# Performance work log

Hardware: AMD Instinct MI355X
Metric: run time of the kernel (lower is better)

Reference implementation:

```python
import jax, jax.numpy as jnp
import numpy as np

B, N, DK, DV = 16, 4096, 64, 64


def setup_inputs() -> dict:
    key = jax.random.key(0)
    kq, kk, kv = jax.random.split(key, 3)
    q = jax.random.normal(kq, (B, N, DK), dtype=jnp.float32)
    k = jax.random.normal(kk, (B, N, DK), dtype=jnp.float32)
    v = jax.random.normal(kv, (B, N, DV), dtype=jnp.float32)
    # causal mask: positions j<=i are attendable (mask==True)
    mask = jnp.tril(jnp.ones((N, N), dtype=bool))[None, :, :]  # (1, N, N)
    return {"q": q, "k": k, "v": v, "mask": mask}


def reference(q, k, v, mask):
    # scores: (B, N, N)
    scale = 1.0 / jnp.sqrt(jnp.asarray(q.shape[-1], dtype=q.dtype))
    scores = jnp.einsum('bnd,bmd->bnm', q, k) * scale
    scores = jnp.where(mask, scores, jnp.asarray(-jnp.inf, dtype=scores.dtype))
    attn = jax.nn.softmax(scores, axis=-1)
    # dropout is identity in eval/reference mode
    return jnp.einsum('bnm,bmd->bnd', attn, v)
```

## Files before the change

### kernel.cpp

```cpp
#include <hip/hip_runtime.h>


#define N_SEQ 4096
#define DIM   64

typedef __bf16  bf16x8 __attribute__((ext_vector_type(8)));
typedef unsigned short u16x8 __attribute__((ext_vector_type(8)));
typedef float   f32x4  __attribute__((ext_vector_type(4)));
typedef short   short4v __attribute__((ext_vector_type(4)));

static __device__ __forceinline__ unsigned short f2bf(float f) {
    unsigned int u = __float_as_uint(f);
    u += 0x7FFFu + ((u >> 16) & 1u);
    return (unsigned short)(u >> 16);
}

static __device__ __forceinline__ unsigned int pk2bf(float a, float b) {
#if defined(__HIP_DEVICE_COMPILE__) && __has_builtin(__builtin_amdgcn_cvt_pk_bf16_f32)
    typedef __bf16 bf16x2_t __attribute__((ext_vector_type(2)));
    bf16x2_t r = __builtin_amdgcn_cvt_pk_bf16_f32(a, b);
    return __builtin_bit_cast(unsigned int, r);
#else
    return (unsigned int)f2bf(a) | ((unsigned int)f2bf(b) << 16);
#endif
}

static __device__ __forceinline__ float fexp2(float x) {
#if defined(__HIP_DEVICE_COMPILE__) && __has_builtin(__builtin_amdgcn_exp2f)
    return __builtin_amdgcn_exp2f(x);
#else
    return exp2f(x);
#endif
}

static __device__ __forceinline__ bf16x8 ld_frag(const void* p) {
    u16x8 u = *reinterpret_cast<const u16x8*>(p);
    return __builtin_bit_cast(bf16x8, u);
}

static __device__ __forceinline__ f32x4 mfma_pv(uint2 a, uint2 b, f32x4 c) {
#if defined(__HIP_DEVICE_COMPILE__)
#if __has_builtin(__builtin_amdgcn_mfma_f32_16x16x16bf16_1k)
    return __builtin_amdgcn_mfma_f32_16x16x16bf16_1k(
        __builtin_bit_cast(short4v, a), __builtin_bit_cast(short4v, b), c, 0, 0, 0);
#else
    f32x4 d;
    asm volatile("v_mfma_f32_16x16x16_bf16 %0, %1, %2, %3"
                 : "=v"(d) : "v"(a), "v"(b), "v"(c));
    return d;
#endif
#else
    (void)a; (void)b;
    return c;
#endif
}

static __device__ __forceinline__ void gl_lds16(const unsigned short* g, unsigned short* l) {
#if defined(__HIP_DEVICE_COMPILE__)
    __builtin_amdgcn_global_load_lds(
        (const __attribute__((address_space(1))) unsigned int*)(g),
        (__attribute__((address_space(3))) unsigned int*)(l), 16, 0, 0);
#else
    (void)g; (void)l;
#endif
}

__global__ __launch_bounds__(256)
void prep_kv(const float* __restrict__ K, const float* __restrict__ V,
             unsigned short* __restrict__ wsK, unsigned short* __restrict__ wsV) {
    const int b = blockIdx.y, t = blockIdx.x;
    if (blockIdx.z == 0) {
        const float* src = K + ((size_t)b * N_SEQ + t * 64) * DIM;
        unsigned short* dst = wsK + ((size_t)(b * 64 + t)) * 4096;
        #pragma unroll
        for (int ph = 0; ph < 2; ++ph) {
            const int gidx = threadIdx.x + ph * 256;
            const int r = gidx >> 3, g = gidx & 7;
            const float* p = src + r * DIM + g * 8;
            f32x4 f0 = *reinterpret_cast<const f32x4*>(p);
            f32x4 f1 = *reinterpret_cast<const f32x4*>(p + 4);
            uint4 w;
            w.x = pk2bf(f0[0], f0[1]); w.y = pk2bf(f0[2], f0[3]);
            w.z = pk2bf(f1[0], f1[1]); w.w = pk2bf(f1[2], f1[3]);
            *reinterpret_cast<uint4*>(&dst[(r * 8 + (g ^ (r & 7))) * 8]) = w;
        }
    } else {
        const int dv = threadIdx.x & 63;
        const int g0 = threadIdx.x >> 6;
        const float* src = V + ((size_t)b * N_SEQ + t * 64) * DIM + dv;
        unsigned short* dst = wsV + ((size_t)(b * 64 + t)) * 4096;
        #pragma unroll
        for (int ph = 0; ph < 2; ++ph) {
            const int gp = g0 + ph * 4;
            float p[8];
            #pragma unroll
            for (int e = 0; e < 8; ++e) {
                const int pos = gp * 8 + e;
                const int kp  = ((pos >> 2) & 3) * 16 + (pos >> 4) * 4 + (pos & 3);
                p[e] = src[(size_t)kp * DIM];
            }
            uint4 w;
            w.x = pk2bf(p[0], p[1]); w.y = pk2bf(p[2], p[3]);
            w.z = pk2bf(p[4], p[5]); w.w = pk2bf(p[6], p[7]);
            *reinterpret_cast<uint4*>(&dst[(dv * 8 + (gp ^ (dv & 7))) * 8]) = w;
        }
    }
}

__global__ __launch_bounds__(256)
void attn_fwd(const float* __restrict__ Q, const unsigned short* __restrict__ wsK,
              const unsigned short* __restrict__ wsV, float* __restrict__ O,
              float* __restrict__ wsO, float* __restrict__ wsL) {
    __shared__ unsigned short kbuf[2][4096];
    __shared__ unsigned short vbuf[2][4096];

    const int tid  = threadIdx.x;
    const int wave = tid >> 6;
    const int lane = tid & 63;
    const int quad = lane >> 4;
    const int ln   = lane & 15;
    const int ln7  = lane & 7;

    const int L    = (int)blockIdx.x;
    const int r    = L & 7;
    const int w    = L >> 3;
    const int role = w & 1;
    const int bsel = (w >> 1) & 1;
    const int j    = w >> 2;
    const int b    = r * 2 + bsel;
    const int T    = 63 - j;

    int it_tile[2], it_k0[2], it_k1[2], it_half[2], n_items;
    if (role == 0) {
        it_tile[0] = j;  it_k0[0] = 0; it_k1[0] = j + 1;  it_half[0] = -1;
        it_tile[1] = T;  it_k0[1] = 0; it_k1[1] = 31 - j; it_half[1] = 0;
        n_items = 2;
    } else {
        it_tile[0] = T;  it_k0[0] = 31 - j; it_k1[0] = 64 - j; it_half[0] = 1;
        n_items = 1;
    }

    int kaddr[2][4];
    #pragma unroll
    for (int s = 0; s < 2; ++s)
        #pragma unroll
        for (int nt = 0; nt < 4; ++nt)
            kaddr[s][nt] = (nt * 16 + ln) * 128 + (((s * 4 + quad) ^ ln7) * 16);
    int vaddr[2][4];
    #pragma unroll
    for (int c = 0; c < 2; ++c)
        #pragma unroll
        for (int dvt = 0; dvt < 4; ++dvt)
            vaddr[c][dvt] = (dvt * 16 + ln) * 128 + ((((quad << 1) | c) ^ ln7) * 16);

    const int dma_off = wave * 1024 + lane * 8;
    const uint2 ones  = make_uint2(0x3F803F80u, 0x3F803F80u);
    const float QS = 0.125f * 1.44269504f;

    const unsigned short* kt_src = wsK + (size_t)b * 64 * 4096;
    const unsigned short* vt_src = wsV + (size_t)b * 64 * 4096;

    for (int it = 0; it < n_items; ++it) {
        const int tt   = it_tile[it];
        const int kt0  = it_k0[it];
        const int kt1  = it_k1[it];
        const int half = it_half[it];
        const int i0   = tt * 64;
        const int qloc = i0 + wave * 16 + ln;

        __syncthreads();

        f32x4 o_acc[4] = {};
        f32x4 lacc = {};

        if (kt0 < kt1) {
            const float* qptr = Q + ((size_t)b * N_SEQ + i0 + wave * 16 + ln) * DIM;
            u16x8 qa[2];
            #pragma unroll
            for (int s = 0; s < 2; ++s) {
                const float* p = qptr + s * 32 + quad * 8;
                f32x4 f0 = *reinterpret_cast<const f32x4*>(p);
                f32x4 f1 = *reinterpret_cast<const f32x4*>(p + 4);
                #pragma unroll
                for (int jj = 0; jj < 4; ++jj) {
                    qa[s][jj]     = f2bf(f0[jj] * QS);
                    qa[s][4 + jj] = f2bf(f1[jj] * QS);
                }
            }

            auto dma = [&](int kt, int bufi) {
                const unsigned short* ks = kt_src + (size_t)kt * 4096 + dma_off;
                const unsigned short* vs = vt_src + (size_t)kt * 4096 + dma_off;
                #pragma unroll
                for (int i = 0; i < 2; ++i) {
                    gl_lds16(ks + i * 512, &kbuf[bufi][wave * 1024 + i * 512]);
                    gl_lds16(vs + i * 512, &vbuf[bufi][wave * 1024 + i * 512]);
                }
            };

            auto compute = [&](int kt, const unsigned short* kb, const unsigned short* vb) {
                f32x4 st[4] = {};
                #pragma unroll
                for (int s = 0; s < 2; ++s) {
                    bf16x8 qf = __builtin_bit_cast(bf16x8, qa[s]);
                    #pragma unroll
                    for (int nt = 0; nt < 4; ++nt) {
                        bf16x8 kf = ld_frag((const char*)kb + kaddr[s][nt]);
                        st[nt] = __builtin_amdgcn_mfma_f32_16x16x32_bf16(kf, qf, st[nt], 0, 0, 0);
                    }
                }
                uint2 pk_d[4];
                if (kt == tt) {
                    const int kbase = kt * 64 + quad * 4;
                    #pragma unroll
                    for (int nt = 0; nt < 4; ++nt) {
                        const int kp = kbase + nt * 16;
                        float p0 = fexp2((kp + 0 > qloc) ? -3.0e38f : st[nt][0]);
                        float p1 = fexp2((kp + 1 > qloc) ? -3.0e38f : st[nt][1]);
                        float p2 = fexp2((kp + 2 > qloc) ? -3.0e38f : st[nt][2]);
                        float p3 = fexp2((kp + 3 > qloc) ? -3.0e38f : st[nt][3]);
                        pk_d[nt].x = pk2bf(p0, p1);
                        pk_d[nt].y = pk2bf(p2, p3);
                    }
                } else {
                    #pragma unroll
                    for (int nt = 0; nt < 4; ++nt) {
                        pk_d[nt].x = pk2bf(fexp2(st[nt][0]), fexp2(st[nt][1]));
                        pk_d[nt].y = pk2bf(fexp2(st[nt][2]), fexp2(st[nt][3]));
                    }
                }
                #pragma unroll
                for (int c = 0; c < 2; ++c)
                    #pragma unroll
                    for (int dvt = 0; dvt < 4; ++dvt) {
                        uint4 bv = *reinterpret_cast<const uint4*>(
                            (const char*)vb + vaddr[c][dvt]);
                        o_acc[dvt] = mfma_pv(pk_d[2 * c],     make_uint2(bv.x, bv.y), o_acc[dvt]);
                        o_acc[dvt] = mfma_pv(pk_d[2 * c + 1], make_uint2(bv.z, bv.w), o_acc[dvt]);
                    }
                #pragma unroll
                for (int nt = 0; nt < 4; ++nt)
                    lacc = mfma_pv(pk_d[nt], ones, lacc);
            };

            dma(kt0, 0);
            int kt = kt0, bufi = 0;
            while (true) {
                __syncthreads();
                if (kt + 1 < kt1) dma(kt + 1, bufi ^ 1);
                compute(kt, kbuf[bufi], vbuf[bufi]);
                if (++kt == kt1) break;
                bufi ^= 1;
            }
        }

        if (half < 0) {
            float* obase = O + ((size_t)b * N_SEQ + i0 + wave * 16) * DIM;
            #pragma unroll
            for (int rr = 0; rr < 4; ++rr) {
                const float inv = 1.0f / lacc[rr];
                #pragma unroll
                for (int dvt = 0; dvt < 4; ++dvt)
                    obase[(quad * 4 + rr) * DIM + dvt * 16 + ln] = o_acc[dvt][rr] * inv;
            }
        } else {
            float* po = wsO + (((size_t)(b * 32 + (tt - 32)) * 2 + half) * 4096)
                      + (wave * 16) * 64;
            float* pl = wsL + (((size_t)(b * 32 + (tt - 32)) * 2 + half) * 64)
                      + wave * 16;
            #pragma unroll
            for (int rr = 0; rr < 4; ++rr) {
                #pragma unroll
                for (int dvt = 0; dvt < 4; ++dvt)
                    po[(quad * 4 + rr) * 64 + dvt * 16 + ln] = o_acc[dvt][rr];
                if (ln == 0) pl[quad * 4 + rr] = lacc[rr];
            }
        }
    }
}

__global__ __launch_bounds__(256)
void norm_out(const float* __restrict__ wsO, const float* __restrict__ wsL,
              float* __restrict__ O) {
    const int t = 32 + blockIdx.x, b = blockIdx.y;
    const int row = threadIdx.x >> 2;
    const int c0  = (threadIdx.x & 3) * 16;
    const size_t base = (size_t)(b * 32 + (t - 32)) * 2;
    const float* p0 = wsO + base * 4096 + row * 64 + c0;
    const float* p1 = p0 + 4096;
    const float* l  = wsL + base * 64;
    const float inv = 1.0f / (l[row] + l[64 + row]);
    float* o = O + ((size_t)b * N_SEQ + t * 64 + row) * 64 + c0;
    #pragma unroll
    for (int i = 0; i < 16; i += 4) {
        f32x4 a = *reinterpret_cast<const f32x4*>(p0 + i);
        f32x4 c = *reinterpret_cast<const f32x4*>(p1 + i);
        f32x4 v = (a + c) * inv;
        *reinterpret_cast<f32x4*>(o + i) = v;
    }
}

extern "C" void kernel_launch(void* const* d_in, const int* in_sizes, int n_in,
                              void* d_out, int out_size, void* d_ws, size_t ws_size,
                              hipStream_t stream) {
    const float* q = (const float*)d_in[0];
    const float* k = (const float*)d_in[1];
    const float* v = (const float*)d_in[2];
    float* out = (float*)d_out;

    unsigned short* wsK = (unsigned short*)d_ws;
    unsigned short* wsV = wsK + (size_t)16 * 64 * 4096;
    float* wsO = (float*)(wsV + (size_t)16 * 64 * 4096);
    float* wsL = wsO + (size_t)16 * 32 * 2 * 4096;

    prep_kv<<<dim3(64, 16, 2), dim3(256), 0, stream>>>(k, v, wsK, wsV);
    attn_fwd<<<dim3(1024), dim3(256), 0, stream>>>(q, wsK, wsV, out, wsO, wsL);
    norm_out<<<dim3(32, 16), dim3(256), 0, stream>>>(wsO, wsL, out);
}
```

Baseline: 193.5 us.

## Split attention tile across waves as 2x2 query/key grid with LDS reduction

Rather than each wave owning 16 query rows against all 64 keys, the four waves form a 2x2 grid: each handles 32 query rows against 32 keys of the tile. Each K fragment loaded from LDS now feeds two MFMAs, and V fragments are halved in size. The V workspace layout and swizzle are changed to match. The partial outputs and row sums from the two key-halves are combined through LDS at the end. This adds two barriers and an LDS reduction per item, and a launch bound hint of 4 blocks per CU constrains registers.

```diff
diff --git a/kernel.cpp b/kernel.cpp
--- a/kernel.cpp
+++ b/kernel.cpp
@@ -88,26 +88,26 @@
         const int dv = threadIdx.x & 63;
         const int g0 = threadIdx.x >> 6;
         const float* src = V + ((size_t)b * N_SEQ + t * 64) * DIM + dv;
-        unsigned short* dst = wsV + ((size_t)(b * 64 + t)) * 4096;
+        unsigned short* dst = wsV + ((size_t)(b * 64 + t)) * 4096 + dv * 64;
         #pragma unroll
         for (int ph = 0; ph < 2; ++ph) {
-            const int gp = g0 + ph * 4;
-            float p[8];
             #pragma unroll
-            for (int e = 0; e < 8; ++e) {
-                const int pos = gp * 8 + e;
-                const int kp  = ((pos >> 2) & 3) * 16 + (pos >> 4) * 4 + (pos & 3);
-                p[e] = src[(size_t)kp * DIM];
+            for (int h = 0; h < 2; ++h) {
+                const int m = g0 * 4 + ph * 2 + h;
+                const float p0 = src[(size_t)(m * 4 + 0) * DIM];
+                const float p1 = src[(size_t)(m * 4 + 1) * DIM];
+                const float p2 = src[(size_t)(m * 4 + 2) * DIM];
+                const float p3 = src[(size_t)(m * 4 + 3) * DIM];
+                uint2 wv;
+                wv.x = pk2bf(p0, p1);
+                wv.y = pk2bf(p2, p3);
+                *reinterpret_cast<uint2*>(&dst[(m ^ (dv & 15)) * 4]) = wv;
             }
-            uint4 w;
-            w.x = pk2bf(p[0], p[1]); w.y = pk2bf(p[2], p[3]);
-            w.z = pk2bf(p[4], p[5]); w.w = pk2bf(p[6], p[7]);
-            *reinterpret_cast<uint4*>(&dst[(dv * 8 + (gp ^ (dv & 7))) * 8]) = w;
         }
     }
 }
 
-__global__ __launch_bounds__(256)
+__global__ __launch_bounds__(256, 4)
 void attn_fwd(const float* __restrict__ Q, const unsigned short* __restrict__ wsK,
               const unsigned short* __restrict__ wsV, float* __restrict__ O,
               float* __restrict__ wsO, float* __restrict__ wsL) {
@@ -120,6 +120,8 @@
     const int quad = lane >> 4;
     const int ln   = lane & 15;
     const int ln7  = lane & 7;
+    const int wq   = wave & 1;
+    const int wk   = wave >> 1;
 
     const int L    = (int)blockIdx.x;
     const int r    = L & 7;
@@ -140,18 +142,19 @@
         n_items = 1;
     }
 
-    int kaddr[2][4];
+    int kaddr[2][2];
     #pragma unroll
     for (int s = 0; s < 2; ++s)
         #pragma unroll
-        for (int nt = 0; nt < 4; ++nt)
-            kaddr[s][nt] = (nt * 16 + ln) * 128 + (((s * 4 + quad) ^ ln7) * 16);
+        for (int nt = 0; nt < 2; ++nt)
+            kaddr[s][nt] = (wk * 32 + nt * 16 + ln) * 128 + (((s * 4 + quad) ^ ln7) * 16);
     int vaddr[2][4];
     #pragma unroll
-    for (int c = 0; c < 2; ++c)
+    for (int nt = 0; nt < 2; ++nt)
         #pragma unroll
         for (int dvt = 0; dvt < 4; ++dvt)
-            vaddr[c][dvt] = (dvt * 16 + ln) * 128 + ((((quad << 1) | c) ^ ln7) * 16);
+            vaddr[nt][dvt] = (dvt * 16 + ln) * 128
+                           + ((((wk * 8 + nt * 4 + quad) ^ ln) & 15) * 8);
 
     const int dma_off = wave * 1024 + lane * 8;
     const uint2 ones  = make_uint2(0x3F803F80u, 0x3F803F80u);
@@ -166,27 +169,28 @@
         const int kt1  = it_k1[it];
         const int half = it_half[it];
         const int i0   = tt * 64;
-        const int qloc = i0 + wave * 16 + ln;
 
         __syncthreads();
 
-        f32x4 o_acc[4] = {};
-        f32x4 lacc = {};
+        f32x4 o_part[2][4] = {};
+        f32x4 lacc[2] = {};
 
         if (kt0 < kt1) {
-            const float* qptr = Q + ((size_t)b * N_SEQ + i0 + wave * 16 + ln) * DIM;
-            u16x8 qa[2];
+            u16x8 qa[2][2];
+            const float* qptr = Q + ((size_t)b * N_SEQ + i0 + wq * 32 + ln) * DIM + quad * 8;
             #pragma unroll
-            for (int s = 0; s < 2; ++s) {
-                const float* p = qptr + s * 32 + quad * 8;
-                f32x4 f0 = *reinterpret_cast<const f32x4*>(p);
-                f32x4 f1 = *reinterpret_cast<const f32x4*>(p + 4);
-                #pragma unroll
-                for (int jj = 0; jj < 4; ++jj) {
-                    qa[s][jj]     = f2bf(f0[jj] * QS);
-                    qa[s][4 + jj] = f2bf(f1[jj] * QS);
-                }
-            }
+            for (int qt = 0; qt < 2; ++qt)
+                #pragma unroll
+                for (int s = 0; s < 2; ++s) {
+                    const float* p = qptr + (size_t)(qt * 16) * DIM + s * 32;
+                    f32x4 f0 = *reinterpret_cast<const f32x4*>(p);
+                    f32x4 f1 = *reinterpret_cast<const f32x4*>(p + 4);
+                    #pragma unroll
+                    for (int jj = 0; jj < 4; ++jj) {
+                        qa[s][qt][jj]     = f2bf(f0[jj] * QS);
+                        qa[s][qt][4 + jj] = f2bf(f1[jj] * QS);
+                    }
+                }
 
             auto dma = [&](int kt, int bufi) {
                 const unsigned short* ks = kt_src + (size_t)kt * 4096 + dma_off;
@@ -199,48 +203,55 @@
             };
 
             auto compute = [&](int kt, const unsigned short* kb, const unsigned short* vb) {
-                f32x4 st[4] = {};
+                f32x4 st[2][2] = {};
                 #pragma unroll
                 for (int s = 0; s < 2; ++s) {
-                    bf16x8 qf = __builtin_bit_cast(bf16x8, qa[s]);
-                    #pragma unroll
-                    for (int nt = 0; nt < 4; ++nt) {
-                        bf16x8 kf = ld_frag((const char*)kb + kaddr[s][nt]);
-                        st[nt] = __builtin_amdgcn_mfma_f32_16x16x32_bf16(kf, qf, st[nt], 0, 0, 0);
-                    }
-                }
-                uint2 pk_d[4];
+                    bf16x8 kf0 = ld_frag((const char*)kb + kaddr[s][0]);
+                    bf16x8 kf1 = ld_frag((const char*)kb + kaddr[s][1]);
+                    #pragma unroll
+                    for (int qt = 0; qt < 2; ++qt) {
+                        bf16x8 qf = __builtin_bit_cast(bf16x8, qa[s][qt]);
+                        st[0][qt] = __builtin_amdgcn_mfma_f32_16x16x32_bf16(kf0, qf, st[0][qt], 0, 0, 0);
+                        st[1][qt] = __builtin_amdgcn_mfma_f32_16x16x32_bf16(kf1, qf, st[1][qt], 0, 0, 0);
+                    }
+                }
+                uint2 pA[2][2];
                 if (kt == tt) {
-                    const int kbase = kt * 64 + quad * 4;
-                    #pragma unroll
-                    for (int nt = 0; nt < 4; ++nt) {
-                        const int kp = kbase + nt * 16;
-                        float p0 = fexp2((kp + 0 > qloc) ? -3.0e38f : st[nt][0]);
-                        float p1 = fexp2((kp + 1 > qloc) ? -3.0e38f : st[nt][1]);
-                        float p2 = fexp2((kp + 2 > qloc) ? -3.0e38f : st[nt][2]);
-                        float p3 = fexp2((kp + 3 > qloc) ? -3.0e38f : st[nt][3]);
-                        pk_d[nt].x = pk2bf(p0, p1);
-                        pk_d[nt].y = pk2bf(p2, p3);
+                    #pragma unroll
+                    for (int nt = 0; nt < 2; ++nt) {
+                        const int kbase = wk * 32 + nt * 16 + quad * 4;
+                        #pragma unroll
+                        for (int qt = 0; qt < 2; ++qt) {
+                            const int qrel = wq * 32 + qt * 16 + ln;
+                            float p0 = fexp2((kbase + 0 > qrel) ? -3.0e38f : st[nt][qt][0]);
+                            float p1 = fexp2((kbase + 1 > qrel) ? -3.0e38f : st[nt][qt][1]);
+                            float p2 = fexp2((kbase + 2 > qrel) ? -3.0e38f : st[nt][qt][2]);
+                            float p3 = fexp2((kbase + 3 > qrel) ? -3.0e38f : st[nt][qt][3]);
+                            pA[nt][qt].x = pk2bf(p0, p1);
+                            pA[nt][qt].y = pk2bf(p2, p3);
+                        }
                     }
                 } else {
                     #pragma unroll
-                    for (int nt = 0; nt < 4; ++nt) {
-                        pk_d[nt].x = pk2bf(fexp2(st[nt][0]), fexp2(st[nt][1]));
-                        pk_d[nt].y = pk2bf(fexp2(st[nt][2]), fexp2(st[nt][3]));
-                    }
-                }
-                #pragma unroll
-                for (int c = 0; c < 2; ++c)
+                    for (int nt = 0; nt < 2; ++nt)
+                        #pragma unroll
+                        for (int qt = 0; qt < 2; ++qt) {
+                            pA[nt][qt].x = pk2bf(fexp2(st[nt][qt][0]), fexp2(st[nt][qt][1]));
+                            pA[nt][qt].y = pk2bf(fexp2(st[nt][qt][2]), fexp2(st[nt][qt][3]));
+                        }
+                }
+                #pragma unroll
+                for (int nt = 0; nt < 2; ++nt) {
                     #pragma unroll
                     for (int dvt = 0; dvt < 4; ++dvt) {
-                        uint4 bv = *reinterpret_cast<const uint4*>(
-                            (const char*)vb + vaddr[c][dvt]);
-                        o_acc[dvt] = mfma_pv(pk_d[2 * c],     make_uint2(bv.x, bv.y), o_acc[dvt]);
-                        o_acc[dvt] = mfma_pv(pk_d[2 * c + 1], make_uint2(bv.z, bv.w), o_acc[dvt]);
-                    }
-                #pragma unroll
-                for (int nt = 0; nt < 4; ++nt)
-                    lacc = mfma_pv(pk_d[nt], ones, lacc);
+                        uint2 bv = *reinterpret_cast<const uint2*>(
+                            (const char*)vb + vaddr[nt][dvt]);
+                        o_part[0][dvt] = mfma_pv(pA[nt][0], bv, o_part[0][dvt]);
+                        o_part[1][dvt] = mfma_pv(pA[nt][1], bv, o_part[1][dvt]);
+                    }
+                    lacc[0] = mfma_pv(pA[nt][0], ones, lacc[0]);
+                    lacc[1] = mfma_pv(pA[nt][1], ones, lacc[1]);
+                }
             };
 
             dma(kt0, 0);
@@ -254,26 +265,62 @@
             }
         }
 
-        if (half < 0) {
-            float* obase = O + ((size_t)b * N_SEQ + i0 + wave * 16) * DIM;
+        __syncthreads();
+        float* red  = reinterpret_cast<float*>(&kbuf[0][0]);
+        float* lred = reinterpret_cast<float*>(&vbuf[0][0]);
+        if (wk == 1) {
             #pragma unroll
-            for (int rr = 0; rr < 4; ++rr) {
-                const float inv = 1.0f / lacc[rr];
+            for (int qt = 0; qt < 2; ++qt) {
                 #pragma unroll
                 for (int dvt = 0; dvt < 4; ++dvt)
-                    obase[(quad * 4 + rr) * DIM + dvt * 16 + ln] = o_acc[dvt][rr] * inv;
+                    #pragma unroll
+                    for (int rr = 0; rr < 4; ++rr)
+                        red[wq * 2048 + qt * 1024 + (quad * 4 + rr) * 64 + dvt * 16 + ln]
+                            = o_part[qt][dvt][rr];
+                if (ln == 0) {
+                    #pragma unroll
+                    for (int rr = 0; rr < 4; ++rr)
+                        lred[wq * 32 + qt * 16 + quad * 4 + rr] = lacc[qt][rr];
+                }
             }
-        } else {
-            float* po = wsO + (((size_t)(b * 32 + (tt - 32)) * 2 + half) * 4096)
-                      + (wave * 16) * 64;
-            float* pl = wsL + (((size_t)(b * 32 + (tt - 32)) * 2 + half) * 64)
-                      + wave * 16;
+        }
+        __syncthreads();
+        if (wk == 0) {
             #pragma unroll
-            for (int rr = 0; rr < 4; ++rr) {
+            for (int qt = 0; qt < 2; ++qt) {
+                f32x4 lt;
+                #pragma unroll
+                for (int rr = 0; rr < 4; ++rr)
+                    lt[rr] = lacc[qt][rr] + lred[wq * 32 + qt * 16 + quad * 4 + rr];
                 #pragma unroll
                 for (int dvt = 0; dvt < 4; ++dvt)
-                    po[(quad * 4 + rr) * 64 + dvt * 16 + ln] = o_acc[dvt][rr];
-                if (ln == 0) pl[quad * 4 + rr] = lacc[rr];
+                    #pragma unroll
+                    for (int rr = 0; rr < 4; ++rr)
+                        o_part[qt][dvt][rr]
+                            += red[wq * 2048 + qt * 1024 + (quad * 4 + rr) * 64 + dvt * 16 + ln];
+
+                const int row0 = wq * 32 + qt * 16 + quad * 4;
+                if (half < 0) {
+                    float* obase = O + ((size_t)b * N_SEQ + i0 + row0) * DIM;
+                    #pragma unroll
+                    for (int rr = 0; rr < 4; ++rr) {
+                        const float inv = 1.0f / lt[rr];
+                        #pragma unroll
+                        for (int dvt = 0; dvt < 4; ++dvt)
+                            obase[rr * DIM + dvt * 16 + ln] = o_part[qt][dvt][rr] * inv;
+                    }
+                } else {
+                    float* po = wsO + (((size_t)(b * 32 + (tt - 32)) * 2 + half) * 4096)
+                              + row0 * 64;
+                    float* pl = wsL + (((size_t)(b * 32 + (tt - 32)) * 2 + half) * 64) + row0;
+                    #pragma unroll
+                    for (int rr = 0; rr < 4; ++rr) {
+                        #pragma unroll
+                        for (int dvt = 0; dvt < 4; ++dvt)
+                            po[rr * 64 + dvt * 16 + ln] = o_part[qt][dvt][rr];
+                        if (ln == 0) pl[rr] = lt[rr];
+                    }
+                }
             }
         }
     }
```

Measured after the change: 196.2 us. About the same (+1.4%).

## Switch attention to 32x32x16 MFMA with 2x2 wave split and LDS reduction

Applied to the files above, without the earlier changes.

Replaces the 16x16 MFMA tiling with 32x32x16 bf16 MFMAs. The four waves now split the 64x64 tile as two query halves times two key halves, and a final LDS reduction combines the key-half partial outputs and row sums. The K/V prep layouts are permuted to match the new fragment addressing, and launch bounds are set to four blocks per CU. The aim is fewer MFMA issues and fewer LDS fragment loads per tile, at the cost of an extra cross-wave reduction with two barriers and higher register pressure from the 16-wide accumulators.

```diff
diff --git a/kernel.cpp b/kernel.cpp
--- a/kernel.cpp
+++ b/kernel.cpp
@@ -7,7 +7,7 @@
 typedef __bf16  bf16x8 __attribute__((ext_vector_type(8)));
 typedef unsigned short u16x8 __attribute__((ext_vector_type(8)));
 typedef float   f32x4  __attribute__((ext_vector_type(4)));
-typedef short   short4v __attribute__((ext_vector_type(4)));
+typedef float   f32x16 __attribute__((ext_vector_type(16)));
 
 static __device__ __forceinline__ unsigned short f2bf(float f) {
     unsigned int u = __float_as_uint(f);
@@ -38,14 +38,13 @@
     return __builtin_bit_cast(bf16x8, u);
 }
 
-static __device__ __forceinline__ f32x4 mfma_pv(uint2 a, uint2 b, f32x4 c) {
+static __device__ __forceinline__ f32x16 mfma32(bf16x8 a, bf16x8 b, f32x16 c) {
 #if defined(__HIP_DEVICE_COMPILE__)
-#if __has_builtin(__builtin_amdgcn_mfma_f32_16x16x16bf16_1k)
-    return __builtin_amdgcn_mfma_f32_16x16x16bf16_1k(
-        __builtin_bit_cast(short4v, a), __builtin_bit_cast(short4v, b), c, 0, 0, 0);
-#else
-    f32x4 d;
-    asm volatile("v_mfma_f32_16x16x16_bf16 %0, %1, %2, %3"
+#if __has_builtin(__builtin_amdgcn_mfma_f32_32x32x16_bf16)
+    return __builtin_amdgcn_mfma_f32_32x32x16_bf16(a, b, c, 0, 0, 0);
+#else
+    f32x16 d;
+    asm volatile("v_mfma_f32_32x32x16_bf16 %0, %1, %2, %3"
                  : "=v"(d) : "v"(a), "v"(b), "v"(c));
     return d;
 #endif
@@ -82,32 +81,30 @@
             uint4 w;
             w.x = pk2bf(f0[0], f0[1]); w.y = pk2bf(f0[2], f0[3]);
             w.z = pk2bf(f1[0], f1[1]); w.w = pk2bf(f1[2], f1[3]);
-            *reinterpret_cast<uint4*>(&dst[(r * 8 + (g ^ (r & 7))) * 8]) = w;
+            const int rp = (r & 51) | ((r & 4) << 1) | ((r & 8) >> 1);
+            *reinterpret_cast<uint4*>(&dst[(rp * 8 + (g ^ (rp & 7))) * 8]) = w;
         }
     } else {
         const int dv = threadIdx.x & 63;
         const int g0 = threadIdx.x >> 6;
         const float* src = V + ((size_t)b * N_SEQ + t * 64) * DIM + dv;
-        unsigned short* dst = wsV + ((size_t)(b * 64 + t)) * 4096;
+        unsigned short* dst = wsV + ((size_t)(b * 64 + t)) * 4096 + dv * 64;
         #pragma unroll
         for (int ph = 0; ph < 2; ++ph) {
-            const int gp = g0 + ph * 4;
+            const int c = g0 * 2 + ph;
             float p[8];
             #pragma unroll
-            for (int e = 0; e < 8; ++e) {
-                const int pos = gp * 8 + e;
-                const int kp  = ((pos >> 2) & 3) * 16 + (pos >> 4) * 4 + (pos & 3);
-                p[e] = src[(size_t)kp * DIM];
-            }
+            for (int e = 0; e < 8; ++e)
+                p[e] = src[(size_t)(c * 8 + e) * DIM];
             uint4 w;
             w.x = pk2bf(p[0], p[1]); w.y = pk2bf(p[2], p[3]);
             w.z = pk2bf(p[4], p[5]); w.w = pk2bf(p[6], p[7]);
-            *reinterpret_cast<uint4*>(&dst[(dv * 8 + (gp ^ (dv & 7))) * 8]) = w;
+            *reinterpret_cast<uint4*>(&dst[(c ^ (dv & 7)) * 8]) = w;
         }
     }
 }
 
-__global__ __launch_bounds__(256)
+__global__ __launch_bounds__(256, 4)
 void attn_fwd(const float* __restrict__ Q, const unsigned short* __restrict__ wsK,
               const unsigned short* __restrict__ wsV, float* __restrict__ O,
               float* __restrict__ wsO, float* __restrict__ wsL) {
@@ -117,9 +114,11 @@
     const int tid  = threadIdx.x;
     const int wave = tid >> 6;
     const int lane = tid & 63;
-    const int quad = lane >> 4;
-    const int ln   = lane & 15;
-    const int ln7  = lane & 7;
+    const int l31  = lane & 31;
+    const int h    = lane >> 5;
+    const int l7   = lane & 7;
+    const int wq   = wave & 1;
+    const int wk   = wave >> 1;
 
     const int L    = (int)blockIdx.x;
     const int r    = L & 7;
@@ -140,21 +139,19 @@
         n_items = 1;
     }
 
-    int kaddr[2][4];
+    int kaddr[4];
     #pragma unroll
-    for (int s = 0; s < 2; ++s)
-        #pragma unroll
-        for (int nt = 0; nt < 4; ++nt)
-            kaddr[s][nt] = (nt * 16 + ln) * 128 + (((s * 4 + quad) ^ ln7) * 16);
-    int vaddr[2][4];
+    for (int s = 0; s < 4; ++s)
+        kaddr[s] = (wk * 32 + l31) * 128 + (((s * 2 + h) ^ l7) * 16);
+    int vbase[2];
     #pragma unroll
-    for (int c = 0; c < 2; ++c)
-        #pragma unroll
-        for (int dvt = 0; dvt < 4; ++dvt)
-            vaddr[c][dvt] = (dvt * 16 + ln) * 128 + ((((quad << 1) | c) ^ ln7) * 16);
+    for (int t = 0; t < 2; ++t)
+        vbase[t] = l31 * 128 + (((wk * 4 + t * 2 + h) ^ l7) * 16);
 
     const int dma_off = wave * 1024 + lane * 8;
-    const uint2 ones  = make_uint2(0x3F803F80u, 0x3F803F80u);
+    const u16x8 ones_u = {0x3F80, 0x3F80, 0x3F80, 0x3F80,
+                          0x3F80, 0x3F80, 0x3F80, 0x3F80};
+    const bf16x8 ones8 = __builtin_bit_cast(bf16x8, ones_u);
     const float QS = 0.125f * 1.44269504f;
 
     const unsigned short* kt_src = wsK + (size_t)b * 64 * 4096;
@@ -166,25 +163,24 @@
         const int kt1  = it_k1[it];
         const int half = it_half[it];
         const int i0   = tt * 64;
-        const int qloc = i0 + wave * 16 + ln;
 
         __syncthreads();
 
-        f32x4 o_acc[4] = {};
-        f32x4 lacc = {};
+        f32x16 o_acc[2] = {};
+        f32x16 lones = {};
 
         if (kt0 < kt1) {
-            const float* qptr = Q + ((size_t)b * N_SEQ + i0 + wave * 16 + ln) * DIM;
-            u16x8 qa[2];
+            u16x8 qb[4];
+            const float* qptr = Q + ((size_t)b * N_SEQ + i0 + wq * 32 + l31) * DIM;
             #pragma unroll
-            for (int s = 0; s < 2; ++s) {
-                const float* p = qptr + s * 32 + quad * 8;
+            for (int s = 0; s < 4; ++s) {
+                const float* p = qptr + s * 16 + h * 8;
                 f32x4 f0 = *reinterpret_cast<const f32x4*>(p);
                 f32x4 f1 = *reinterpret_cast<const f32x4*>(p + 4);
                 #pragma unroll
                 for (int jj = 0; jj < 4; ++jj) {
-                    qa[s][jj]     = f2bf(f0[jj] * QS);
-                    qa[s][4 + jj] = f2bf(f1[jj] * QS);
+                    qb[s][jj]     = f2bf(f0[jj] * QS);
+                    qb[s][4 + jj] = f2bf(f1[jj] * QS);
                 }
             }
 
@@ -199,48 +195,42 @@
             };
 
             auto compute = [&](int kt, const unsigned short* kb, const unsigned short* vb) {
-                f32x4 st[4] = {};
-                #pragma unroll
-                for (int s = 0; s < 2; ++s) {
-                    bf16x8 qf = __builtin_bit_cast(bf16x8, qa[s]);
-                    #pragma unroll
-                    for (int nt = 0; nt < 4; ++nt) {
-                        bf16x8 kf = ld_frag((const char*)kb + kaddr[s][nt]);
-                        st[nt] = __builtin_amdgcn_mfma_f32_16x16x32_bf16(kf, qf, st[nt], 0, 0, 0);
-                    }
-                }
-                uint2 pk_d[4];
+                f32x16 st = {};
+                #pragma unroll
+                for (int s = 0; s < 4; ++s) {
+                    bf16x8 kf = ld_frag((const char*)kb + kaddr[s]);
+                    st = mfma32(kf, __builtin_bit_cast(bf16x8, qb[s]), st);
+                }
+                float pex[16];
                 if (kt == tt) {
-                    const int kbase = kt * 64 + quad * 4;
-                    #pragma unroll
-                    for (int nt = 0; nt < 4; ++nt) {
-                        const int kp = kbase + nt * 16;
-                        float p0 = fexp2((kp + 0 > qloc) ? -3.0e38f : st[nt][0]);
-                        float p1 = fexp2((kp + 1 > qloc) ? -3.0e38f : st[nt][1]);
-                        float p2 = fexp2((kp + 2 > qloc) ? -3.0e38f : st[nt][2]);
-                        float p3 = fexp2((kp + 3 > qloc) ? -3.0e38f : st[nt][3]);
-                        pk_d[nt].x = pk2bf(p0, p1);
-                        pk_d[nt].y = pk2bf(p2, p3);
+                    const int qth = wq * 32 + l31 - 8 * h - wk * 32;
+                    #pragma unroll
+                    for (int rr = 0; rr < 16; ++rr) {
+                        const int K0 = (rr & 7) | ((rr & 8) << 1);
+                        pex[rr] = fexp2((K0 > qth) ? -3.0e38f : st[rr]);
                     }
                 } else {
                     #pragma unroll
-                    for (int nt = 0; nt < 4; ++nt) {
-                        pk_d[nt].x = pk2bf(fexp2(st[nt][0]), fexp2(st[nt][1]));
-                        pk_d[nt].y = pk2bf(fexp2(st[nt][2]), fexp2(st[nt][3]));
+                    for (int rr = 0; rr < 16; ++rr)
+                        pex[rr] = fexp2(st[rr]);
+                }
+                unsigned int u[8];
+                #pragma unroll
+                for (int g = 0; g < 4; ++g) {
+                    u[2 * g]     = pk2bf(pex[4 * g],     pex[4 * g + 1]);
+                    u[2 * g + 1] = pk2bf(pex[4 * g + 2], pex[4 * g + 3]);
+                }
+                #pragma unroll
+                for (int t = 0; t < 2; ++t) {
+                    uint4 aw = make_uint4(u[4 * t], u[4 * t + 1], u[4 * t + 2], u[4 * t + 3]);
+                    bf16x8 pa = __builtin_bit_cast(bf16x8, aw);
+                    #pragma unroll
+                    for (int dvt = 0; dvt < 2; ++dvt) {
+                        bf16x8 bv = ld_frag((const char*)vb + vbase[t] + dvt * 4096);
+                        o_acc[dvt] = mfma32(pa, bv, o_acc[dvt]);
                     }
-                }
-                #pragma unroll
-                for (int c = 0; c < 2; ++c)
-                    #pragma unroll
-                    for (int dvt = 0; dvt < 4; ++dvt) {
-                        uint4 bv = *reinterpret_cast<const uint4*>(
-                            (const char*)vb + vaddr[c][dvt]);
-                        o_acc[dvt] = mfma_pv(pk_d[2 * c],     make_uint2(bv.x, bv.y), o_acc[dvt]);
-                        o_acc[dvt] = mfma_pv(pk_d[2 * c + 1], make_uint2(bv.z, bv.w), o_acc[dvt]);
-                    }
-                #pragma unroll
-                for (int nt = 0; nt < 4; ++nt)
-                    lacc = mfma_pv(pk_d[nt], ones, lacc);
+                    lones = mfma32(pa, ones8, lones);
+                }
             };
 
             dma(kt0, 0);
@@ -254,26 +244,48 @@
             }
         }
 
-        if (half < 0) {
-            float* obase = O + ((size_t)b * N_SEQ + i0 + wave * 16) * DIM;
+        __syncthreads();
+        float* red  = reinterpret_cast<float*>(&kbuf[0][0]);
+        float* lred = reinterpret_cast<float*>(&vbuf[0][0]);
+        if (wk == 1) {
             #pragma unroll
-            for (int rr = 0; rr < 4; ++rr) {
-                const float inv = 1.0f / lacc[rr];
-                #pragma unroll
-                for (int dvt = 0; dvt < 4; ++dvt)
-                    obase[(quad * 4 + rr) * DIM + dvt * 16 + ln] = o_acc[dvt][rr] * inv;
+            for (int rr = 0; rr < 16; ++rr) {
+                const int qrow = (rr & 3) + 8 * (rr >> 2) + 4 * h;
+                #pragma unroll
+                for (int dvt = 0; dvt < 2; ++dvt)
+                    red[wq * 2048 + qrow * 64 + dvt * 32 + l31] = o_acc[dvt][rr];
+                if (l31 == 0) lred[wq * 32 + qrow] = lones[rr];
             }
-        } else {
-            float* po = wsO + (((size_t)(b * 32 + (tt - 32)) * 2 + half) * 4096)
-                      + (wave * 16) * 64;
-            float* pl = wsL + (((size_t)(b * 32 + (tt - 32)) * 2 + half) * 64)
-                      + wave * 16;
-            #pragma unroll
-            for (int rr = 0; rr < 4; ++rr) {
-                #pragma unroll
-                for (int dvt = 0; dvt < 4; ++dvt)
-                    po[(quad * 4 + rr) * 64 + dvt * 16 + ln] = o_acc[dvt][rr];
-                if (ln == 0) pl[quad * 4 + rr] = lacc[rr];
+        }
+        __syncthreads();
+        if (wk == 0) {
+            if (half < 0) {
+                float* obase = O + ((size_t)b * N_SEQ + i0 + wq * 32) * DIM;
+                #pragma unroll
+                for (int rr = 0; rr < 16; ++rr) {
+                    const int qrow = (rr & 3) + 8 * (rr >> 2) + 4 * h;
+                    const float lt = lones[rr] + lred[wq * 32 + qrow];
+                    const float inv = 1.0f / lt;
+                    #pragma unroll
+                    for (int dvt = 0; dvt < 2; ++dvt) {
+                        const float val = o_acc[dvt][rr]
+                            + red[wq * 2048 + qrow * 64 + dvt * 32 + l31];
+                        obase[qrow * DIM + dvt * 32 + l31] = val * inv;
+                    }
+                }
+            } else {
+                float* po = wsO + (((size_t)(b * 32 + (tt - 32)) * 2 + half) * 4096);
+                float* pl = wsL + (((size_t)(b * 32 + (tt - 32)) * 2 + half) * 64);
+                #pragma unroll
+                for (int rr = 0; rr < 16; ++rr) {
+                    const int qrow = (rr & 3) + 8 * (rr >> 2) + 4 * h;
+                    const float lt = lones[rr] + lred[wq * 32 + qrow];
+                    #pragma unroll
+                    for (int dvt = 0; dvt < 2; ++dvt)
+                        po[(wq * 32 + qrow) * 64 + dvt * 32 + l31] = o_acc[dvt][rr]
+                            + red[wq * 2048 + qrow * 64 + dvt * 32 + l31];
+                    if (l31 == 0) pl[wq * 32 + qrow] = lt;
+                }
             }
         }
     }
```

Result: slower. 222.2 us (+14.8%).
